# Kernel tuning notes

Hardware: AMD Instinct MI355X
Metric: run time of the kernel (lower is better)

## Reference

```python
import jax, jax.numpy as jnp
import numpy as np

BOX_SIZE = 120
RESOLUTION = 1.0
NUM_NEIGHBOURS = 2
NUM_TYPES = 11
MAX_ATOMS = 512
BATCH = 4


def setup_inputs() -> dict:
    key = jax.random.key(0)
    k1, k2 = jax.random.split(key)
    # coords uniformly inside the box with a margin so Gaussians stay mostly in-grid
    margin = 5.0
    input_coords = jax.random.uniform(
        k1, (BATCH, NUM_TYPES, 3 * MAX_ATOMS), dtype=jnp.float32,
        minval=margin, maxval=BOX_SIZE * RESOLUTION - margin)
    num_atoms = jax.random.randint(k2, (BATCH, NUM_TYPES), 1, MAX_ATOMS + 1).astype(jnp.int64)
    return {"input_coords": input_coords, "num_atoms": num_atoms}


def _coords2volume(input_coords, num_atoms):
    B, T, C = input_coords.shape
    A = C // 3
    pos = input_coords.reshape(B * T, A, 3)  # [BT, A, 3] xyz per atom
    n = NUM_NEIGHBOURS
    res = RESOLUTION
    # (2n+1)^3 neighbour-cell offsets
    r = jnp.arange(-n, n + 1)
    offs = jnp.stack(jnp.meshgrid(r, r, r, indexing="ij"), axis=-1).reshape(-1, 3)  # [K,3]
    # home cell of each atom (spatial hash cell)
    cell = jnp.floor(pos / res).astype(jnp.int32)  # [BT, A, 3]
    nb = cell[:, :, None, :] + offs[None, None, :, :]  # [BT, A, K, 3]
    # truncated Gaussian density at neighbour-cell grid points
    cell_pos = nb.astype(pos.dtype) * res
    r2 = jnp.sum((cell_pos - pos[:, :, None, :]) ** 2, axis=-1)  # [BT, A, K]
    val = jnp.exp(-r2 / (res * res))
    # mask cells outside the grid and padded atoms
    in_box = jnp.all((nb >= 0) & (nb < BOX_SIZE), axis=-1)  # [BT, A, K]
    atom_mask = jnp.arange(A)[None, :] < num_atoms.reshape(-1)[:, None]  # [BT, A]
    val = jnp.where(in_box & atom_mask[:, :, None], val, 0.0)
    # scatter-add into flattened voxel grid
    flat = (nb[..., 0] * BOX_SIZE + nb[..., 1]) * BOX_SIZE + nb[..., 2]
    flat = jnp.clip(flat, 0, BOX_SIZE ** 3 - 1)
    vol = jnp.zeros((B * T, BOX_SIZE ** 3), dtype=pos.dtype)
    bidx = jnp.arange(B * T)[:, None, None]
    vol = vol.at[bidx, flat].add(val)
    return vol.reshape(B, T, BOX_SIZE, BOX_SIZE, BOX_SIZE)


def reference(input_coords, num_atoms):
    return _coords2volume(input_coords, num_atoms)
```

## Files before the change

kernel.cpp:

```cpp
#include <hip/hip_runtime.h>

#define BOX 120
#define BOX3 (BOX * BOX * BOX)
#define NTYPES 11
#define NBATCH 4
#define BT (NBATCH * NTYPES)
#define MAXA 512
#define NNB 2
#define KCELLS 125

__global__ __launch_bounds__(256)
void zero_out_kernel(float4* __restrict__ out, int n4) {
    int i = blockIdx.x * blockDim.x + threadIdx.x;
    if (i < n4) out[i] = make_float4(0.f, 0.f, 0.f, 0.f);
}

__global__ __launch_bounds__(256)
void TypedCoords2Volume_scatter(const float* __restrict__ coords,
                                const int* __restrict__ num_atoms,
                                float* __restrict__ out) {
    int idx = blockIdx.x * blockDim.x + threadIdx.x;
    const int total = BT * MAXA * KCELLS;
    if (idx >= total) return;

    int k   = idx % KCELLS;
    int tmp = idx / KCELLS;
    int a   = tmp % MAXA;
    int bt  = tmp / MAXA;

    int na = num_atoms[bt];
    if (a >= na) return;

    const float* p = coords + (size_t)bt * (3 * MAXA) + (size_t)a * 3;
    float px = p[0];
    float py = p[1];
    float pz = p[2];

    int cx = (int)floorf(px);
    int cy = (int)floorf(py);
    int cz = (int)floorf(pz);

    int dz = k % 5;
    int t2 = k / 5;
    int dy = t2 % 5;
    int dx = t2 / 5;

    int nx = cx + dx - NNB;
    int ny = cy + dy - NNB;
    int nz = cz + dz - NNB;

    if ((unsigned)nx >= BOX || (unsigned)ny >= BOX || (unsigned)nz >= BOX) return;

    float fx = (float)nx - px;
    float fy = (float)ny - py;
    float fz = (float)nz - pz;
    float r2 = fx * fx + fy * fy + fz * fz;
    float val = __expf(-r2);

    size_t off = (size_t)bt * BOX3 + (size_t)((nx * BOX + ny) * BOX + nz);
    atomicAdd(out + off, val);
}

extern "C" void kernel_launch(void* const* d_in, const int* in_sizes, int n_in,
                              void* d_out, int out_size, void* d_ws, size_t ws_size,
                              hipStream_t stream) {
    const float* coords    = (const float*)d_in[0];
    const int*   num_atoms = (const int*)d_in[1];
    float*       out       = (float*)d_out;

    int n4 = out_size / 4;
    {
        const int block = 256;
        const int grid  = (n4 + block - 1) / block;
        zero_out_kernel<<<grid, block, 0, stream>>>((float4*)d_out, n4);
    }

    const int total  = BT * MAXA * KCELLS;
    const int block  = 256;
    const int grid   = (total + block - 1) / block;
    TypedCoords2Volume_scatter<<<grid, block, 0, stream>>>(coords, num_atoms, out);
}
```

Measured before the change: 330.2 us.

## Replace atomic scatter with per-column atom binning and output-stationary gather

Atoms are first binned by their (x,y) home cell into a fixed-capacity workspace table. Each gather block then covers one x-plane and 8 y-rows, loads the nearby atoms into shared memory, and computes every voxel's density directly. Every output element is written exactly once with non-temporal stores, so the separate full-volume zeroing pass and the global float atomics go away. The costs are extra small kernels and a hard per-bin capacity of 8 atoms, which silently drops atoms in crowded bins. The old scatter path is kept as a fallback when the workspace is too small.

```diff
diff --git a/kernel.cpp b/kernel.cpp
--- a/kernel.cpp
+++ b/kernel.cpp
@@ -1,6 +1,8 @@
 #include <hip/hip_runtime.h>
+#include <stdint.h>
 
 #define BOX 120
+#define BOX2 (BOX * BOX)
 #define BOX3 (BOX * BOX * BOX)
 #define NTYPES 11
 #define NBATCH 4
@@ -9,6 +11,104 @@
 #define NNB 2
 #define KCELLS 125
 
+#define NBINS (BT * BOX2)
+#define BINCAP 8
+#define YTILE 8
+#define NYT (BOX / YTILE)
+
+#define WS_COUNTS_BYTES ((size_t)NBINS * 4)
+#define WS_BINS_BYTES   ((size_t)NBINS * BINCAP * 2)
+#define WS_NEEDED       (WS_COUNTS_BYTES + WS_BINS_BYTES)
+
+
+__global__ __launch_bounds__(256)
+void zero_counts_kernel(uint4* __restrict__ counts4, int n4) {
+    int i = blockIdx.x * blockDim.x + threadIdx.x;
+    if (i < n4) counts4[i] = make_uint4(0u, 0u, 0u, 0u);
+}
+
+__global__ __launch_bounds__(256)
+void bin_kernel(const float* __restrict__ coords,
+                const int* __restrict__ num_atoms,
+                uint32_t* __restrict__ counts,
+                uint16_t* __restrict__ bins) {
+    int tid = blockIdx.x * blockDim.x + threadIdx.x;
+    if (tid >= BT * MAXA) return;
+    int bt = tid / MAXA;
+    int a  = tid % MAXA;
+    if (a >= num_atoms[bt]) return;
+    const float* p = coords + (size_t)bt * (3 * MAXA) + (size_t)a * 3;
+    int cx = (int)floorf(p[0]);
+    int cy = (int)floorf(p[1]);
+    if ((unsigned)cx >= BOX || (unsigned)cy >= BOX) return;
+    int bin = (bt * BOX + cx) * BOX + cy;
+    uint32_t idx = atomicAdd(&counts[bin], 1u);
+    if (idx < BINCAP) bins[(size_t)bin * BINCAP + idx] = (uint16_t)a;
+}
+
+__global__ __launch_bounds__(256)
+void gather_kernel(const float* __restrict__ coords,
+                   const uint32_t* __restrict__ counts,
+                   const uint16_t* __restrict__ bins,
+                   float* __restrict__ out) {
+    int b  = blockIdx.x;
+    int bt = b / (BOX * NYT);
+    int r  = b % (BOX * NYT);
+    int x  = r / NYT;
+    int y0 = (r % NYT) * YTILE;
+
+    const int NB_Y = YTILE + 2 * NNB;
+    __shared__ float4 s_at[5 * NB_Y * BINCAP];
+    __shared__ float  s_w[5 * NB_Y * BINCAP];
+    __shared__ int    s_n;
+    if (threadIdx.x == 0) s_n = 0;
+    __syncthreads();
+
+    int t = threadIdx.x;
+    if (t < 5 * NB_Y) {
+        int cxb = x - NNB + t / NB_Y;
+        int cyb = y0 - NNB + t % NB_Y;
+        if ((unsigned)cxb < BOX && (unsigned)cyb < BOX) {
+            int bin = (bt * BOX + cxb) * BOX + cyb;
+            int c = (int)counts[bin];
+            if (c > BINCAP) c = BINCAP;
+            if (c > 0) {
+                int base = atomicAdd(&s_n, c);
+                for (int k = 0; k < c; ++k) {
+                    int a = bins[(size_t)bin * BINCAP + k];
+                    const float* p = coords + (size_t)bt * (3 * MAXA) + (size_t)a * 3;
+                    float px = p[0], py = p[1], pz = p[2];
+                    float fx = (float)x - px;
+                    s_at[base + k] = make_float4(py, pz, floorf(py), floorf(pz));
+                    s_w[base + k]  = __expf(-fx * fx);
+                }
+            }
+        }
+    }
+    __syncthreads();
+    int n = s_n;
+
+    size_t obase = (size_t)(bt * BOX + x) * BOX2 + (size_t)y0 * BOX;
+    for (int it = 0; it < 4; ++it) {
+        int v = threadIdx.x + it * 256;
+        if (v < YTILE * BOX) {
+            float yf = (float)(y0 + v / BOX);
+            float zf = (float)(v % BOX);
+            float acc = 0.f;
+            for (int i = 0; i < n; ++i) {
+                float4 at = s_at[i];
+                if (fabsf(yf - at.z) <= 2.0f && fabsf(zf - at.w) <= 2.0f) {
+                    float dy = yf - at.x;
+                    float dz = zf - at.y;
+                    acc += s_w[i] * __expf(-(dy * dy + dz * dz));
+                }
+            }
+            __builtin_nontemporal_store(acc, out + obase + v);
+        }
+    }
+}
+
+
 __global__ __launch_bounds__(256)
 void zero_out_kernel(float4* __restrict__ out, int n4) {
     int i = blockIdx.x * blockDim.x + threadIdx.x;
@@ -16,49 +116,28 @@
 }
 
 __global__ __launch_bounds__(256)
-void TypedCoords2Volume_scatter(const float* __restrict__ coords,
-                                const int* __restrict__ num_atoms,
-                                float* __restrict__ out) {
+void scatter_kernel(const float* __restrict__ coords,
+                    const int* __restrict__ num_atoms,
+                    float* __restrict__ out) {
     int idx = blockIdx.x * blockDim.x + threadIdx.x;
     const int total = BT * MAXA * KCELLS;
     if (idx >= total) return;
-
     int k   = idx % KCELLS;
     int tmp = idx / KCELLS;
     int a   = tmp % MAXA;
     int bt  = tmp / MAXA;
-
-    int na = num_atoms[bt];
-    if (a >= na) return;
-
+    if (a >= num_atoms[bt]) return;
     const float* p = coords + (size_t)bt * (3 * MAXA) + (size_t)a * 3;
-    float px = p[0];
-    float py = p[1];
-    float pz = p[2];
-
-    int cx = (int)floorf(px);
-    int cy = (int)floorf(py);
-    int cz = (int)floorf(pz);
-
-    int dz = k % 5;
-    int t2 = k / 5;
-    int dy = t2 % 5;
-    int dx = t2 / 5;
-
-    int nx = cx + dx - NNB;
-    int ny = cy + dy - NNB;
-    int nz = cz + dz - NNB;
-
+    float px = p[0], py = p[1], pz = p[2];
+    int dz = k % 5, t2 = k / 5;
+    int dy = t2 % 5, dx = t2 / 5;
+    int nx = (int)floorf(px) + dx - NNB;
+    int ny = (int)floorf(py) + dy - NNB;
+    int nz = (int)floorf(pz) + dz - NNB;
     if ((unsigned)nx >= BOX || (unsigned)ny >= BOX || (unsigned)nz >= BOX) return;
-
-    float fx = (float)nx - px;
-    float fy = (float)ny - py;
-    float fz = (float)nz - pz;
-    float r2 = fx * fx + fy * fy + fz * fz;
-    float val = __expf(-r2);
-
-    size_t off = (size_t)bt * BOX3 + (size_t)((nx * BOX + ny) * BOX + nz);
-    atomicAdd(out + off, val);
+    float fx = (float)nx - px, fy = (float)ny - py, fz = (float)nz - pz;
+    float val = __expf(-(fx * fx + fy * fy + fz * fz));
+    atomicAdd(out + (size_t)bt * BOX3 + (size_t)((nx * BOX + ny) * BOX + nz), val);
 }
 
 extern "C" void kernel_launch(void* const* d_in, const int* in_sizes, int n_in,
@@ -68,15 +147,21 @@
     const int*   num_atoms = (const int*)d_in[1];
     float*       out       = (float*)d_out;
 
-    int n4 = out_size / 4;
-    {
-        const int block = 256;
-        const int grid  = (n4 + block - 1) / block;
-        zero_out_kernel<<<grid, block, 0, stream>>>((float4*)d_out, n4);
+    if (ws_size >= WS_NEEDED) {
+        uint32_t* counts = (uint32_t*)d_ws;
+        uint16_t* bins   = (uint16_t*)((char*)d_ws + WS_COUNTS_BYTES);
+
+        int n4 = NBINS / 4;
+        zero_counts_kernel<<<(n4 + 255) / 256, 256, 0, stream>>>((uint4*)counts, n4);
+
+        bin_kernel<<<(BT * MAXA + 255) / 256, 256, 0, stream>>>(coords, num_atoms, counts, bins);
+
+        int gblocks = BT * BOX * NYT;
+        gather_kernel<<<gblocks, 256, 0, stream>>>(coords, counts, bins, out);
+    } else {
+        int n4 = out_size / 4;
+        zero_out_kernel<<<(n4 + 255) / 256, 256, 0, stream>>>((float4*)d_out, n4);
+        const int total = BT * MAXA * KCELLS;
+        scatter_kernel<<<(total + 255) / 256, 256, 0, stream>>>(coords, num_atoms, out);
     }
-
-    const int total  = BT * MAXA * KCELLS;
-    const int block  = 256;
-    const int grid   = (total + block - 1) / block;
-    TypedCoords2Volume_scatter<<<grid, block, 0, stream>>>(coords, num_atoms, out);
 }
```

Measured after the change: 354.6 us. +7.4%, slower.
